# Kernel tuning notes

Hardware: AMD Instinct MI355X
Metric: run time of the kernel (lower is better)

The kernel has to match this reference:

```python
import jax, jax.numpy as jnp
import numpy as np

D = 1024      # EMBEDDING_DIM
H = 16        # ATTENTION_HEADS
HD = 64       # HEAD_DIM
B, S = 4, 2048
EPS = 1e-5


def setup_inputs() -> dict:
    key = jax.random.key(0)
    ks = jax.random.split(key, 16)
    std = 0.02
    inp = {
        "x": jax.random.normal(ks[0], (B, S, D), dtype=jnp.float32),
        # per-head Q/K/V weights stacked: [H, D, HD]
        "Wq": jax.random.normal(ks[1], (H, D, HD), dtype=jnp.float32) * std,
        "Wk": jax.random.normal(ks[2], (H, D, HD), dtype=jnp.float32) * std,
        "Wv": jax.random.normal(ks[3], (H, D, HD), dtype=jnp.float32) * std,
        "bq": jnp.zeros((H, HD), dtype=jnp.float32),
        "bk": jnp.zeros((H, HD), dtype=jnp.float32),
        "bv": jnp.zeros((H, HD), dtype=jnp.float32),
        "Wo": jax.random.normal(ks[4], (D, D), dtype=jnp.float32) * std,
        "bo": jnp.zeros((D,), dtype=jnp.float32),
        "W1": jax.random.normal(ks[5], (D, 4 * D), dtype=jnp.float32) * std,
        "b1": jnp.zeros((4 * D,), dtype=jnp.float32),
        "W2": jax.random.normal(ks[6], (4 * D, D), dtype=jnp.float32) * std,
        "b2": jnp.zeros((D,), dtype=jnp.float32),
        # single shared LayerNorm (same module used for both pre-norms)
        "gamma": jnp.ones((D,), dtype=jnp.float32),
        "beta": jnp.zeros((D,), dtype=jnp.float32),
    }
    return inp


def _layer_norm(x, gamma, beta):
    mu = jnp.mean(x, axis=-1, keepdims=True)
    var = jnp.mean(jnp.square(x - mu), axis=-1, keepdims=True)
    return (x - mu) * jax.lax.rsqrt(var + EPS) * gamma + beta


def _block(x, Wq, Wk, Wv, bq, bk, bv, Wo, bo, W1, b1, W2, b2, gamma, beta):
    # pre-norm attention
    h = _layer_norm(x, gamma, beta)                     # [B,S,D]
    Q = jnp.einsum('bsd,hdk->bhsk', h, Wq) + bq[None, :, None, :]
    K = jnp.einsum('bsd,hdk->bhsk', h, Wk) + bk[None, :, None, :]
    V = jnp.einsum('bsd,hdk->bhsk', h, Wv) + bv[None, :, None, :]
    scores = jnp.einsum('bhsk,bhtk->bhst', Q, K) / jnp.sqrt(jnp.float32(HD))
    causal = jnp.tril(jnp.ones((S, S), dtype=bool))     # True = keep
    scores = jnp.where(causal[None, None], scores, -jnp.inf)
    attn = jax.nn.softmax(scores, axis=-1)              # [B,H,S,S]
    out = jnp.einsum('bhst,bhtk->bhsk', attn, V)        # [B,H,S,HD]
    out = out.transpose(0, 2, 1, 3).reshape(x.shape[0], x.shape[1], D)
    x = x + out @ Wo + bo
    # pre-norm MLP (shared layer norm params)
    h2 = _layer_norm(x, gamma, beta)
    mlp = jax.nn.gelu(h2 @ W1 + b1, approximate=False) @ W2 + b2
    return x + mlp


def reference(x, Wq, Wk, Wv, bq, bk, bv, Wo, bo, W1, b1, W2, b2, gamma, beta):
    return _block(x, Wq, Wk, Wv, bq, bk, bv, Wo, bo, W1, b1, W2, b2, gamma, beta)
```

## Files before the change

kernel.cpp:

```cpp
#include <hip/hip_runtime.h>
#include <hip/hip_bf16.h>

typedef __bf16  bf16x8 __attribute__((ext_vector_type(8)));
typedef float   f32x4  __attribute__((ext_vector_type(4)));
typedef short   s16x8  __attribute__((ext_vector_type(8)));

typedef const __attribute__((address_space(1))) void g_void;
typedef __attribute__((address_space(3))) void l_void;

__device__ __forceinline__ short f2b(float x) {
    __hip_bfloat16 h = __float2bfloat16(x);
    return __builtin_bit_cast(short, h);
}

__device__ __forceinline__ int pk2(float lo, float hi) {
    return (int)(unsigned short)f2b(lo) | ((int)f2b(hi) << 16);
}

__device__ __forceinline__ float fast_gelu(float v) {
    const float a = fminf(2.3022082f * (v + 0.044715f * v * v * v), 126.0f);
    const float t = exp2f(a);
    return v * t / (t + 1.0f);
}

__device__ __forceinline__ f32x4 mfma16(s16x8 a, s16x8 b, f32x4 c) {
    return __builtin_amdgcn_mfma_f32_16x16x32_bf16(
        __builtin_bit_cast(bf16x8, a), __builtin_bit_cast(bf16x8, b), c, 0, 0, 0);
}

__global__ __launch_bounds__(256) void transpose_bf16(
    const float* __restrict__ src, short* __restrict__ dst, int R, int C) {
    __shared__ float tile[32][33];
    src += (size_t)blockIdx.z * R * C;
    dst += (size_t)blockIdx.z * R * C;
    const int c0 = blockIdx.x * 32, r0 = blockIdx.y * 32;
    const int tx = threadIdx.x & 31, ty = threadIdx.x >> 5;
#pragma unroll
    for (int i = 0; i < 32; i += 8)
        tile[ty + i][tx] = src[(size_t)(r0 + ty + i) * C + c0 + tx];
    __syncthreads();
#pragma unroll
    for (int i = 0; i < 32; i += 8)
        dst[(size_t)(c0 + ty + i) * R + r0 + tx] = f2b(tile[tx][ty + i]);
}

__global__ __launch_bounds__(256) void concat_bias(
    const float* __restrict__ bq, const float* __restrict__ bk,
    const float* __restrict__ bv, float* __restrict__ o) {
    int i = blockIdx.x * 256 + threadIdx.x;
    if (i < 1024)      o[i] = bq[i];
    else if (i < 2048) o[i] = bk[i - 1024];
    else if (i < 3072) o[i] = bv[i - 2048];
}

__global__ __launch_bounds__(256) void ln_bf16(
    const float* __restrict__ x, const float* __restrict__ gamma,
    const float* __restrict__ beta, short* __restrict__ out) {
    __shared__ float red[8];
    const int row = blockIdx.x, tid = threadIdx.x;
    const float4 v = *(const float4*)(x + (size_t)row * 1024 + tid * 4);
    float s = v.x + v.y + v.z + v.w;
    float q = v.x * v.x + v.y * v.y + v.z * v.z + v.w * v.w;
#pragma unroll
    for (int off = 32; off > 0; off >>= 1) {
        s += __shfl_xor(s, off);
        q += __shfl_xor(q, off);
    }
    if ((tid & 63) == 0) { red[(tid >> 6) * 2] = s; red[(tid >> 6) * 2 + 1] = q; }
    __syncthreads();
    s = red[0] + red[2] + red[4] + red[6];
    q = red[1] + red[3] + red[5] + red[7];
    const float mu = s * (1.0f / 1024.0f);
    const float var = q * (1.0f / 1024.0f) - mu * mu;
    const float rs = rsqrtf(var + 1e-5f);
    const float4 g  = *(const float4*)(gamma + tid * 4);
    const float4 bt = *(const float4*)(beta + tid * 4);
    short4 o;
    o.x = f2b((v.x - mu) * rs * g.x + bt.x);
    o.y = f2b((v.y - mu) * rs * g.y + bt.y);
    o.z = f2b((v.z - mu) * rs * g.z + bt.z);
    o.w = f2b((v.w - mu) * rs * g.w + bt.w);
    *(short4*)(out + (size_t)row * 1024 + tid * 4) = o;
}

template <int MODE, int SWZ>
__global__ __launch_bounds__(512) void gemm_bf16(
    const short* __restrict__ A, const short* __restrict__ Bt,
    const float* __restrict__ bias, const float* __restrict__ resid,
    float* __restrict__ outf, short* __restrict__ outb, short* __restrict__ vt,
    int M, int N, int K) {
    __shared__ __align__(16) short As[2 * 128 * 32];
    __shared__ __align__(16) short Bs[2 * 128 * 32];

    const int tid = threadIdx.x;
    const int wave = tid >> 6, lane = tid & 63;
    const int l16 = lane & 15, quad = lane >> 4;
    const int wm = wave & 3, wn = wave >> 2;
    const int gx = gridDim.x;
    const int g = blockIdx.y * gx + blockIdx.x;
    const int xcd = g & 7, s = g >> 3;
    int m0, n0;
    if (SWZ == 0) {
        const int nband = gx >> 3;
        const int sm = s / nband;
        const int sn = s - sm * nband;
        m0 = sm * 128;
        n0 = (xcd * nband + sn) * 128;
    } else {
        const int mband = gridDim.y >> 3;
        const int sm = s / gx;
        m0 = (xcd * mband + sm) * 128;
        n0 = (s - sm * gx) * 128;
    }
    const int lrow = lane >> 2;
    const int lcol = (lane & 3) * 8;

    f32x4 acc[2][4] = {};

    for (int kk = 0; kk < K; kk += 64) {
#pragma unroll
        for (int p = 0; p < 2; ++p) {
            const int r = wave * 16 + lrow;
            const short* ga = A + (size_t)(m0 + r) * K + kk + p * 32 + lcol;
            short* la = &As[p * 4096 + wave * 512];
            __builtin_amdgcn_global_load_lds((g_void*)ga, (l_void*)la, 16, 0, 0);
            const short* gb = Bt + (size_t)(n0 + r) * K + kk + p * 32 + lcol;
            short* lb = &Bs[p * 4096 + wave * 512];
            __builtin_amdgcn_global_load_lds((g_void*)gb, (l_void*)lb, 16, 0, 0);
        }
        __syncthreads();
#pragma unroll
        for (int p = 0; p < 2; ++p) {
            s16x8 a[2], b[4];
#pragma unroll
            for (int t = 0; t < 2; ++t)
                a[t] = *(const s16x8*)&As[p * 4096 + (wm * 32 + t * 16 + l16) * 32 + quad * 8];
#pragma unroll
            for (int t = 0; t < 4; ++t)
                b[t] = *(const s16x8*)&Bs[p * 4096 + (wn * 64 + t * 16 + l16) * 32 + quad * 8];
#pragma unroll
            for (int mt = 0; mt < 2; ++mt)
#pragma unroll
                for (int nt = 0; nt < 4; ++nt)
                    acc[mt][nt] = mfma16(a[mt], b[nt], acc[mt][nt]);
        }
        __syncthreads();
    }

#pragma unroll
    for (int mt = 0; mt < 2; ++mt) {
#pragma unroll
        for (int nt = 0; nt < 4; ++nt) {
            const int row = m0 + wm * 32 + mt * 16 + quad * 4;
            const int col = n0 + wn * 64 + nt * 16 + l16;
            const float bc = bias[col];
            float v[4];
#pragma unroll
            for (int r = 0; r < 4; ++r) v[r] = acc[mt][nt][r] + bc;

            if (MODE == 0) {
                const int sel = col >> 10, within = col & 1023;
                const int h = within >> 6, hd = within & 63;
                const size_t bidx = (size_t)row >> 11, sp = row & 2047;
                if (sel == 0) {
#pragma unroll
                    for (int r = 0; r < 4; ++r) v[r] *= 0.18033688011112042f;
                }
                if (sel < 2) {
#pragma unroll
                    for (int r = 0; r < 4; ++r)
                        outb[(size_t)sel * (8192ull * 1024) +
                             ((bidx * 16 + h) * 2048 + sp + r) * 64 + hd] = f2b(v[r]);
                } else {
                    short4 o4;
                    o4.x = f2b(v[0]); o4.y = f2b(v[1]);
                    o4.z = f2b(v[2]); o4.w = f2b(v[3]);
                    *(short4*)&vt[((bidx * 16 + h) * 64 + hd) * 2048 + sp] = o4;
                }
            } else if (MODE == 1) {
#pragma unroll
                for (int r = 0; r < 4; ++r) {
                    const size_t rr = (size_t)(row + r);
                    outf[rr * N + col] = v[r] + resid[rr * N + col];
                }
            } else {
#pragma unroll
                for (int r = 0; r < 4; ++r)
                    outb[(size_t)(row + r) * N + col] = f2b(fast_gelu(v[r]));
            }
        }
    }
}

__global__ __launch_bounds__(256) void attn_kernel(
    const short* __restrict__ Q, const short* __restrict__ K,
    const short* __restrict__ Vt, short* __restrict__ O) {
    const int bid = blockIdx.x;
    const int xcd = bid & 7;
    const int sub = (bid >> 3) & 7;
    const int grp = bid >> 6;
    const int bh  = grp * 8 + xcd;
    const int h = bh & 15, b = bh >> 4;
    const int gq = sub;
    const int tid = threadIdx.x, wave = tid >> 6, lane = tid & 63;
    const int l16 = lane & 15, quad = lane >> 4;

    __shared__ __align__(16) short Ks[2][64 * 72];
    __shared__ __align__(16) short Vts[2][64 * 72];
    __shared__ __align__(16) short Ps[4][16 * 72];

    const size_t bhoff = (size_t)bh * (2048ull * 64);
    const int srow = tid >> 2;
    const int sseg = (tid & 3) * 16;

    const int qts[4] = {gq, 15 - gq, 16 + gq, 31 - gq};

    for (int pass = 0; pass < 4; ++pass) {
        const int qt = qts[pass];
        const int q0 = qt * 64;
        const int q_lane = q0 + wave * 16 + l16;

        const short* qrow = Q + bhoff + (size_t)q_lane * 64;
        s16x8 bq0 = *(const s16x8*)(qrow + quad * 8);
        s16x8 bq1 = *(const s16x8*)(qrow + 32 + quad * 8);

        f32x4 oacc[4] = {};
        float lsum = 0.0f;

        s16x8 k0, k1, v0, v1;
        {
            const short* kg = K + bhoff + (size_t)srow * 64 + sseg;
            k0 = *(const s16x8*)kg;
            k1 = *(const s16x8*)(kg + 8);
            const short* vg = Vt + bhoff + (size_t)srow * 2048 + sseg;
            v0 = *(const s16x8*)vg;
            v1 = *(const s16x8*)(vg + 8);
        }

        for (int j = 0; j <= qt; ++j) {
            const int buf = j & 1;
            *(s16x8*)&Ks[buf][srow * 72 + sseg]      = k0;
            *(s16x8*)&Ks[buf][srow * 72 + sseg + 8]  = k1;
            *(s16x8*)&Vts[buf][srow * 72 + sseg]     = v0;
            *(s16x8*)&Vts[buf][srow * 72 + sseg + 8] = v1;
            __syncthreads();

            if (j < qt) {
                const short* kg = K + bhoff + (size_t)((j + 1) * 64 + srow) * 64 + sseg;
                k0 = *(const s16x8*)kg;
                k1 = *(const s16x8*)(kg + 8);
                const short* vg = Vt + bhoff + (size_t)srow * 2048 + (j + 1) * 64 + sseg;
                v0 = *(const s16x8*)vg;
                v1 = *(const s16x8*)(vg + 8);
            }

            f32x4 st[4];
#pragma unroll
            for (int s = 0; s < 4; ++s) {
                s16x8 ak0 = *(const s16x8*)&Ks[buf][(s * 16 + l16) * 72 + quad * 8];
                s16x8 ak1 = *(const s16x8*)&Ks[buf][(s * 16 + l16) * 72 + 32 + quad * 8];
                f32x4 c = {};
                c = mfma16(ak0, bq0, c);
                c = mfma16(ak1, bq1, c);
                st[s] = c;
            }
            if (j == qt) {
#pragma unroll
                for (int s = 0; s < 4; ++s)
#pragma unroll
                    for (int r = 0; r < 4; ++r) {
                        const int t = j * 64 + s * 16 + quad * 4 + r;
                        if (t > q_lane) st[s][r] = -3000.0f;
                    }
            }
            float rs = 0.0f;
#pragma unroll
            for (int s = 0; s < 4; ++s) {
#pragma unroll
                for (int r = 0; r < 4; ++r) {
                    st[s][r] = exp2f(st[s][r]);
                    rs += st[s][r];
                }
                int2 pw;
                pw.x = pk2(st[s][0], st[s][1]);
                pw.y = pk2(st[s][2], st[s][3]);
                *(int2*)&Ps[wave][l16 * 72 + s * 16 + quad * 4] = pw;
            }
            rs += __shfl_xor(rs, 16);
            rs += __shfl_xor(rs, 32);
            lsum += rs;

            asm volatile("s_waitcnt lgkmcnt(0)" ::: "memory");
            s16x8 ap0 = *(const s16x8*)&Ps[wave][l16 * 72 + quad * 8];
            s16x8 ap1 = *(const s16x8*)&Ps[wave][l16 * 72 + 32 + quad * 8];

#pragma unroll
            for (int nt = 0; nt < 4; ++nt) {
                s16x8 bv0 = *(const s16x8*)&Vts[buf][(nt * 16 + l16) * 72 + quad * 8];
                s16x8 bv1 = *(const s16x8*)&Vts[buf][(nt * 16 + l16) * 72 + 32 + quad * 8];
                oacc[nt] = mfma16(ap0, bv0, oacc[nt]);
                oacc[nt] = mfma16(ap1, bv1, oacc[nt]);
            }
        }
        __syncthreads();

        float inv[4];
#pragma unroll
        for (int r = 0; r < 4; ++r)
            inv[r] = 1.0f / __shfl(lsum, quad * 4 + r, 64);
#pragma unroll
        for (int nt = 0; nt < 4; ++nt)
#pragma unroll
            for (int r = 0; r < 4; ++r) {
                const int row = q0 + wave * 16 + quad * 4 + r;
                O[((size_t)b * 2048 + row) * 1024 + h * 64 + nt * 16 + l16] =
                    f2b(oacc[nt][r] * inv[r]);
            }
    }
}

extern "C" void kernel_launch(void* const* d_in, const int* in_sizes, int n_in,
                              void* d_out, int out_size, void* d_ws, size_t ws_size,
                              hipStream_t stream) {
    const float* x     = (const float*)d_in[0];
    const float* Wq    = (const float*)d_in[1];
    const float* Wk    = (const float*)d_in[2];
    const float* Wv    = (const float*)d_in[3];
    const float* bq    = (const float*)d_in[4];
    const float* bk    = (const float*)d_in[5];
    const float* bv    = (const float*)d_in[6];
    const float* Wo    = (const float*)d_in[7];
    const float* bo    = (const float*)d_in[8];
    const float* W1    = (const float*)d_in[9];
    const float* b1    = (const float*)d_in[10];
    const float* W2    = (const float*)d_in[11];
    const float* b2    = (const float*)d_in[12];
    const float* gamma = (const float*)d_in[13];
    const float* beta  = (const float*)d_in[14];
    float* out = (float*)d_out;

    char* ws = (char*)d_ws;
    size_t off = 0;
    auto alloc = [&](size_t bytes) -> char* {
        char* p = ws + off;
        off += (bytes + 255) & ~(size_t)255;
        return p;
    };
    short* h1    = (short*)alloc(8192ull * 1024 * 2);
    short* btqkv = (short*)alloc(3072ull * 1024 * 2);
    short* btwo  = (short*)alloc(1024ull * 1024 * 2);
    short* btw1  = (short*)alloc(4096ull * 1024 * 2);
    short* btw2  = (short*)alloc(1024ull * 4096 * 2);
    float* bqkv  = (float*)alloc(3072ull * 4);
    short* qkv   = (short*)alloc(2ull * 8192 * 1024 * 2);
    short* vt    = (short*)alloc(8192ull * 1024 * 2);
    short* aout  = (short*)alloc(8192ull * 1024 * 2);
    float* x2    = (float*)alloc(8192ull * 1024 * 4);
    short* h2    = (short*)alloc(8192ull * 1024 * 2);
    short* m1    = (short*)alloc(8192ull * 4096 * 2);

    transpose_bf16<<<dim3(2, 32, 16), 256, 0, stream>>>(Wq, btqkv, 1024, 64);
    transpose_bf16<<<dim3(2, 32, 16), 256, 0, stream>>>(Wk, btqkv + 1024ull * 1024, 1024, 64);
    transpose_bf16<<<dim3(2, 32, 16), 256, 0, stream>>>(Wv, btqkv + 2ull * 1024 * 1024, 1024, 64);
    transpose_bf16<<<dim3(32, 32, 1), 256, 0, stream>>>(Wo, btwo, 1024, 1024);
    transpose_bf16<<<dim3(128, 32, 1), 256, 0, stream>>>(W1, btw1, 1024, 4096);
    transpose_bf16<<<dim3(32, 128, 1), 256, 0, stream>>>(W2, btw2, 4096, 1024);
    concat_bias<<<12, 256, 0, stream>>>(bq, bk, bv, bqkv);

    ln_bf16<<<8192, 256, 0, stream>>>(x, gamma, beta, h1);
    gemm_bf16<0, 0><<<dim3(24, 64), 512, 0, stream>>>(
        h1, btqkv, bqkv, nullptr, nullptr, qkv, vt, 8192, 3072, 1024);
    attn_kernel<<<512, 256, 0, stream>>>(
        qkv, qkv + 8192ull * 1024, vt, aout);
    gemm_bf16<1, 0><<<dim3(8, 64), 512, 0, stream>>>(
        aout, btwo, bo, x, x2, nullptr, nullptr, 8192, 1024, 1024);
    ln_bf16<<<8192, 256, 0, stream>>>(x2, gamma, beta, h2);
    gemm_bf16<2, 0><<<dim3(32, 64), 512, 0, stream>>>(
        h2, btw1, b1, nullptr, nullptr, m1, nullptr, 8192, 4096, 1024);
    gemm_bf16<1, 1><<<dim3(8, 64), 512, 0, stream>>>(
        m1, btw2, b2, x2, out, nullptr, nullptr, 8192, 1024, 4096);
}
```

Before: 504.7 us.

## Add 256x256-tile pipelined GEMM kernel for QKV and MLP up-projection

Adds a new gemm256 kernel that computes 256x256 output tiles per 512-thread workgroup with 8x4 MFMA fragments per wave. It double-buffers A/B tiles in LDS using direct global-to-LDS loads with an XOR swizzle, and interleaves loads with MFMA phases using barriers and s_setprio. Workgroup ids are remapped across XCDs. The QKV projection and the W1+GELU GEMM now use it, aiming at more data reuse and better latency hiding, at the cost of higher register/LDS pressure and a fragile hand-scheduled pipeline.

```diff
diff --git a/kernel.cpp b/kernel.cpp
--- a/kernel.cpp
+++ b/kernel.cpp
@@ -158,6 +158,177 @@
 #pragma unroll
             for (int r = 0; r < 4; ++r) v[r] = acc[mt][nt][r] + bc;
 
+            if (MODE == 1) {
+#pragma unroll
+                for (int r = 0; r < 4; ++r) {
+                    const size_t rr = (size_t)(row + r);
+                    outf[rr * N + col] = v[r] + resid[rr * N + col];
+                }
+            } else {
+#pragma unroll
+                for (int r = 0; r < 4; ++r)
+                    outb[(size_t)(row + r) * N + col] = f2b(fast_gelu(v[r]));
+            }
+        }
+    }
+}
+
+
+#define MM(MH, NH, AF, BB)                                                   \
+    _Pragma("unroll") for (int p = 0; p < 2; ++p)                            \
+        _Pragma("unroll") for (int ii = 0; ii < 4; ++ii)                     \
+            _Pragma("unroll") for (int jj = 0; jj < 2; ++jj)                 \
+                acc[(MH) * 4 + ii][(NH) * 2 + jj] =                          \
+                    mfma16(AF[ii][p], BB[jj][p],                             \
+                           acc[(MH) * 4 + ii][(NH) * 2 + jj]);
+
+#define PH_MID                                                               \
+    __builtin_amdgcn_s_barrier();                                            \
+    __builtin_amdgcn_s_setprio(1);
+
+#define PH_END                                                               \
+    __builtin_amdgcn_s_setprio(0);                                           \
+    __builtin_amdgcn_sched_barrier(0);                                       \
+    __builtin_amdgcn_s_barrier();                                            \
+    __builtin_amdgcn_sched_barrier(0);
+
+#define KTILE(BUF, S1, S2, S3, S4)                                           \
+    {                                                                        \
+        s16x8 af[4][2], bl[2][2], bh[2][2];                                  \
+                                                     \
+        _Pragma("unroll") for (int ii = 0; ii < 4; ++ii)                     \
+            _Pragma("unroll") for (int p = 0; p < 2; ++p)                    \
+                af[ii][p] = LDA(BUF, ii, p);                                 \
+        _Pragma("unroll") for (int jj = 0; jj < 2; ++jj)                     \
+            _Pragma("unroll") for (int p = 0; p < 2; ++p)                    \
+                bl[jj][p] = LDB(BUF, jj, p);                                 \
+        S1;                                                                  \
+        PH_MID;                                                              \
+        MM(0, 0, af, bl);                                                    \
+        PH_END;                                                              \
+                                                     \
+        _Pragma("unroll") for (int jj = 0; jj < 2; ++jj)                     \
+            _Pragma("unroll") for (int p = 0; p < 2; ++p)                    \
+                bh[jj][p] = LDB(BUF, 2 + jj, p);                             \
+        S2;                                                                  \
+        PH_MID;                                                              \
+        MM(0, 1, af, bh);                                                    \
+        PH_END;                                                              \
+                                                     \
+        _Pragma("unroll") for (int ii = 0; ii < 4; ++ii)                     \
+            _Pragma("unroll") for (int p = 0; p < 2; ++p)                    \
+                af[ii][p] = LDA(BUF, 4 + ii, p);                             \
+        S3;                                                                  \
+        PH_MID;                                                              \
+        MM(1, 1, af, bh);                                                    \
+        PH_END;                                                              \
+                                      \
+        S4;                                                                  \
+        asm volatile("s_waitcnt vmcnt(4)" ::: "memory");                     \
+        PH_MID;                                                              \
+        MM(1, 0, af, bl);                                                    \
+        PH_END;                                                              \
+    }
+
+template <int MODE>
+__global__ __launch_bounds__(512, 2) void gemm256(
+    const short* __restrict__ A, const short* __restrict__ Bt,
+    const float* __restrict__ bias, const float* __restrict__ resid,
+    float* __restrict__ outf, short* __restrict__ outb, short* __restrict__ vt,
+    int M, int N, int K) {
+    __shared__ __align__(16) short As[32768];
+    __shared__ __align__(16) short Bs[32768];
+
+    const int tid = threadIdx.x;
+    const int wave = tid >> 6, lane = tid & 63;
+    const int l16 = lane & 15, quad = lane >> 4;
+    const int wm = wave >> 2, wn = wave & 3;
+
+    const int nwg = gridDim.x;
+    const int g = blockIdx.x;
+    const int wgid = (g & 7) * (nwg >> 3) + (g >> 3);
+    const int mtiles = M >> 8;
+    const int m0 = (wgid % mtiles) << 8;
+    const int n0 = (wgid / mtiles) << 8;
+
+    const int rc = l16 * 32 + ((quad * 8) ^ ((l16 >> 3) << 4));
+    const int a_rd = wm * 8192 + rc;
+    const int b_rd = (wn >> 1) * 8192 + (wn & 1) * 4096 + rc;
+
+    auto LDA = [&](int buf, int i, int p) {
+        return *(const s16x8*)&As[buf * 16384 + a_rd + (i * 2 + p) * 512];
+    };
+    auto LDB = [&](int buf, int j, int p) {
+        return *(const s16x8*)&Bs[buf * 16384 + b_rd + (j * 2 + p) * 512];
+    };
+
+    int r0, c0, r1, c1;
+    {
+        int s = tid * 16;
+        int lin = s ^ (((s >> 9) & 1) << 5);
+        r0 = ((lin >> 11) << 4) + ((lin >> 6) & 15);
+        c0 = (((lin >> 10) & 1) << 5) + ((lin & 63) >> 1);
+        s = (tid + 512) * 16;
+        lin = s ^ (((s >> 9) & 1) << 5);
+        r1 = ((lin >> 11) << 4) + ((lin >> 6) & 15);
+        c1 = (((lin >> 10) & 1) << 5) + ((lin & 63) >> 1);
+    }
+
+    const short* gA = A + (size_t)m0 * K;
+    const short* gB = Bt + (size_t)n0 * K;
+
+    auto STAGE = [&](const short* gbase, int half, int kk, short* lds) {
+        const short* s0 = gbase + (size_t)(half * 128 + r0) * K + kk + c0;
+        const short* s1 = gbase + (size_t)(half * 128 + r1) * K + kk + c1;
+        short* d0 = lds + half * 8192 + wave * 512;
+        short* d1 = lds + half * 8192 + 4096 + wave * 512;
+        __builtin_amdgcn_global_load_lds((g_void*)s0, (l_void*)d0, 16, 0, 0);
+        __builtin_amdgcn_global_load_lds((g_void*)s1, (l_void*)d1, 16, 0, 0);
+    };
+
+    f32x4 acc[8][4] = {};
+
+    STAGE(gA, 0, 0, As);
+    STAGE(gA, 1, 0, As);
+    STAGE(gB, 0, 0, Bs);
+    STAGE(gB, 1, 0, Bs);
+    STAGE(gB, 0, 64, Bs + 16384);
+    STAGE(gB, 1, 64, Bs + 16384);
+    asm volatile("s_waitcnt vmcnt(4)" ::: "memory");
+    __builtin_amdgcn_s_barrier();
+    __builtin_amdgcn_sched_barrier(0);
+
+    const int NI = K >> 7;
+    for (int it = 0; it < NI; ++it) {
+        const int kA1 = (2 * it + 1) * 64;
+        int kn0 = (2 * it + 2) * 64;
+        if (kn0 > K - 64) kn0 = K - 64;
+        int kn1 = (2 * it + 3) * 64;
+        if (kn1 > K - 64) kn1 = K - 64;
+
+        KTILE(0,
+              STAGE(gA, 0, kA1, As + 16384),
+              STAGE(gA, 1, kA1, As + 16384),
+              STAGE(gB, 0, kn0, Bs),
+              STAGE(gB, 1, kn0, Bs));
+        KTILE(1,
+              STAGE(gA, 0, kn0, As),
+              STAGE(gA, 1, kn0, As),
+              STAGE(gB, 0, kn1, Bs + 16384),
+              STAGE(gB, 1, kn1, Bs + 16384));
+    }
+
+#pragma unroll
+    for (int i = 0; i < 8; ++i) {
+#pragma unroll
+        for (int j = 0; j < 4; ++j) {
+            const int row = m0 + wm * 128 + i * 16 + quad * 4;
+            const int col = n0 + wn * 64 + j * 16 + l16;
+            const float bc = bias[col];
+            float v[4];
+#pragma unroll
+            for (int r = 0; r < 4; ++r) v[r] = acc[i][j][r] + bc;
+
             if (MODE == 0) {
                 const int sel = col >> 10, within = col & 1023;
                 const int h = within >> 6, hd = within & 63;
@@ -191,6 +362,11 @@
         }
     }
 }
+
+#undef KTILE
+#undef PH_MID
+#undef PH_END
+#undef MM
 
 __global__ __launch_bounds__(256) void attn_kernel(
     const short* __restrict__ Q, const short* __restrict__ K,
@@ -368,14 +544,14 @@
     concat_bias<<<12, 256, 0, stream>>>(bq, bk, bv, bqkv);
 
     ln_bf16<<<8192, 256, 0, stream>>>(x, gamma, beta, h1);
-    gemm_bf16<0, 0><<<dim3(24, 64), 512, 0, stream>>>(
+    gemm256<0><<<384, 512, 0, stream>>>(
         h1, btqkv, bqkv, nullptr, nullptr, qkv, vt, 8192, 3072, 1024);
     attn_kernel<<<512, 256, 0, stream>>>(
         qkv, qkv + 8192ull * 1024, vt, aout);
     gemm_bf16<1, 0><<<dim3(8, 64), 512, 0, stream>>>(
         aout, btwo, bo, x, x2, nullptr, nullptr, 8192, 1024, 1024);
     ln_bf16<<<8192, 256, 0, stream>>>(x2, gamma, beta, h2);
-    gemm_bf16<2, 0><<<dim3(32, 64), 512, 0, stream>>>(
+    gemm256<2><<<512, 512, 0, stream>>>(
         h2, btw1, b1, nullptr, nullptr, m1, nullptr, 8192, 4096, 1024);
     gemm_bf16<1, 1><<<dim3(8, 64), 512, 0, stream>>>(
         m1, btw2, b2, x2, out, nullptr, nullptr, 8192, 1024, 4096);
```

Measured after the change: 531.1 us. 1.05x slower.

## Add 256x256 bf16 GEMM with direct-to-LDS loads for QKV and MLP-up

Applied to the files above, without the earlier changes.

Adds a new GEMM kernel that computes 256x256 output tiles per 512-thread workgroup. It loads A and B straight from global memory into LDS, double-buffers the K loop, and software-pipelines inline-asm ds_read_b128 fragment loads against MFMA chains with wave priority raised during the MFMA bursts. Block indices are remapped so that consecutive tiles are spread over XCDs. The QKV projection and the first MLP GEMM now use this kernel, aiming for more operand reuse and better latency hiding; the cost is 128KB of LDS per block, limiting occupancy to one block per CU, plus hand-tuned waitcnt logic that is fragile.

```diff
diff --git a/kernel.cpp b/kernel.cpp
--- a/kernel.cpp
+++ b/kernel.cpp
@@ -4,6 +4,7 @@
 typedef __bf16  bf16x8 __attribute__((ext_vector_type(8)));
 typedef float   f32x4  __attribute__((ext_vector_type(4)));
 typedef short   s16x8  __attribute__((ext_vector_type(8)));
+typedef int     i32x4  __attribute__((ext_vector_type(4)));
 
 typedef const __attribute__((address_space(1))) void g_void;
 typedef __attribute__((address_space(3))) void l_void;
@@ -27,6 +28,8 @@
     return __builtin_amdgcn_mfma_f32_16x16x32_bf16(
         __builtin_bit_cast(bf16x8, a), __builtin_bit_cast(bf16x8, b), c, 0, 0, 0);
 }
+
+#define S16(x) __builtin_bit_cast(s16x8, x)
 
 __global__ __launch_bounds__(256) void transpose_bf16(
     const float* __restrict__ src, short* __restrict__ dst, int R, int C) {
@@ -158,6 +161,197 @@
 #pragma unroll
             for (int r = 0; r < 4; ++r) v[r] = acc[mt][nt][r] + bc;
 
+            if (MODE == 1) {
+#pragma unroll
+                for (int r = 0; r < 4; ++r) {
+                    const size_t rr = (size_t)(row + r);
+                    outf[rr * N + col] = v[r] + resid[rr * N + col];
+                }
+            } else {
+#pragma unroll
+                for (int r = 0; r < 4; ++r)
+                    outb[(size_t)(row + r) * N + col] = f2b(fast_gelu(v[r]));
+            }
+        }
+    }
+}
+
+
+#define DSR(dst, b, o)                                                       \
+    asm volatile("ds_read_b128 %0, %1 offset:" #o : "=v"(dst) : "v"(b))
+
+#define LGKM12                                                               \
+    asm volatile("s_waitcnt lgkmcnt(12)" ::: "memory");                      \
+    __builtin_amdgcn_sched_barrier(0)
+
+#define MM32(A, B)                                                           \
+    acc[0][0]=mfma16(S16(A##0),S16(B##0),acc[0][0]);                         \
+    acc[0][1]=mfma16(S16(A##0),S16(B##1),acc[0][1]);                         \
+    acc[0][2]=mfma16(S16(A##0),S16(B##2),acc[0][2]);                         \
+    acc[0][3]=mfma16(S16(A##0),S16(B##3),acc[0][3]);                         \
+    acc[1][0]=mfma16(S16(A##1),S16(B##0),acc[1][0]);                         \
+    acc[1][1]=mfma16(S16(A##1),S16(B##1),acc[1][1]);                         \
+    acc[1][2]=mfma16(S16(A##1),S16(B##2),acc[1][2]);                         \
+    acc[1][3]=mfma16(S16(A##1),S16(B##3),acc[1][3]);                         \
+    acc[2][0]=mfma16(S16(A##2),S16(B##0),acc[2][0]);                         \
+    acc[2][1]=mfma16(S16(A##2),S16(B##1),acc[2][1]);                         \
+    acc[2][2]=mfma16(S16(A##2),S16(B##2),acc[2][2]);                         \
+    acc[2][3]=mfma16(S16(A##2),S16(B##3),acc[2][3]);                         \
+    acc[3][0]=mfma16(S16(A##3),S16(B##0),acc[3][0]);                         \
+    acc[3][1]=mfma16(S16(A##3),S16(B##1),acc[3][1]);                         \
+    acc[3][2]=mfma16(S16(A##3),S16(B##2),acc[3][2]);                         \
+    acc[3][3]=mfma16(S16(A##3),S16(B##3),acc[3][3]);                         \
+    acc[4][0]=mfma16(S16(A##4),S16(B##0),acc[4][0]);                         \
+    acc[4][1]=mfma16(S16(A##4),S16(B##1),acc[4][1]);                         \
+    acc[4][2]=mfma16(S16(A##4),S16(B##2),acc[4][2]);                         \
+    acc[4][3]=mfma16(S16(A##4),S16(B##3),acc[4][3]);                         \
+    acc[5][0]=mfma16(S16(A##5),S16(B##0),acc[5][0]);                         \
+    acc[5][1]=mfma16(S16(A##5),S16(B##1),acc[5][1]);                         \
+    acc[5][2]=mfma16(S16(A##5),S16(B##2),acc[5][2]);                         \
+    acc[5][3]=mfma16(S16(A##5),S16(B##3),acc[5][3]);                         \
+    acc[6][0]=mfma16(S16(A##6),S16(B##0),acc[6][0]);                         \
+    acc[6][1]=mfma16(S16(A##6),S16(B##1),acc[6][1]);                         \
+    acc[6][2]=mfma16(S16(A##6),S16(B##2),acc[6][2]);                         \
+    acc[6][3]=mfma16(S16(A##6),S16(B##3),acc[6][3]);                         \
+    acc[7][0]=mfma16(S16(A##7),S16(B##0),acc[7][0]);                         \
+    acc[7][1]=mfma16(S16(A##7),S16(B##1),acc[7][1]);                         \
+    acc[7][2]=mfma16(S16(A##7),S16(B##2),acc[7][2]);                         \
+    acc[7][3]=mfma16(S16(A##7),S16(B##3),acc[7][3])
+
+#define READ_P0(SA, SB, AR, BR)                                              \
+    DSR(SB##0, BR, 0);    DSR(SB##1, BR, 2048);                              \
+    DSR(SB##2, BR, 4096); DSR(SB##3, BR, 6144);                              \
+    DSR(SA##0, AR, 0);    DSR(SA##1, AR, 2048);                              \
+    DSR(SA##2, AR, 4096); DSR(SA##3, AR, 6144);                              \
+    DSR(SA##4, AR, 8192); DSR(SA##5, AR, 10240);                             \
+    DSR(SA##6, AR, 12288); DSR(SA##7, AR, 14336)
+
+#define READ_P1(SA, SB, AR, BR)                                              \
+    DSR(SB##0, BR, 1024); DSR(SB##1, BR, 3072);                              \
+    DSR(SB##2, BR, 5120); DSR(SB##3, BR, 7168);                              \
+    DSR(SA##0, AR, 1024); DSR(SA##1, AR, 3072);                              \
+    DSR(SA##2, AR, 5120); DSR(SA##3, AR, 7168);                              \
+    DSR(SA##4, AR, 9216); DSR(SA##5, AR, 11264);                             \
+    DSR(SA##6, AR, 13312); DSR(SA##7, AR, 15360)
+
+#define TILE(ARc, BRc, ARn, BRn, BUFB)                                       \
+    READ_P1(ga, gb, ARc, BRc);                                               \
+    LGKM12;                                                                  \
+    __builtin_amdgcn_s_setprio(1);                                           \
+    MM32(fa, fb);                                                            \
+    __builtin_amdgcn_s_setprio(0);                                           \
+    __builtin_amdgcn_sched_barrier(0);                                       \
+    READ_P0(fa, fb, ARn, BRn);                                               \
+    LGKM12;                                                                  \
+    STAGE8(BUFB);                                                            \
+    __builtin_amdgcn_s_setprio(1);                                           \
+    MM32(ga, gb);                                                            \
+    __builtin_amdgcn_s_setprio(0);                                           \
+    __builtin_amdgcn_sched_barrier(0);                                       \
+    ADV();                                                                   \
+    asm volatile("s_waitcnt vmcnt(8)" ::: "memory");                         \
+    __builtin_amdgcn_s_barrier();                                            \
+    __builtin_amdgcn_sched_barrier(0)
+
+template <int MODE>
+__global__ __launch_bounds__(512, 2) void gemm256(
+    const short* __restrict__ A, const short* __restrict__ Bt,
+    const float* __restrict__ bias, const float* __restrict__ resid,
+    float* __restrict__ outf, short* __restrict__ outb, short* __restrict__ vt,
+    int M, int N, int K) {
+    __shared__ __align__(16) short As[32768];
+    __shared__ __align__(16) short Bs[32768];
+
+    const int tid = threadIdx.x;
+    const int wave = tid >> 6, lane = tid & 63;
+    const int l16 = lane & 15, quad = lane >> 4;
+    const int wm = wave >> 2, wn = wave & 3;
+
+    const int nwg = gridDim.x;
+    const int g = blockIdx.x;
+    const int wgid = (g & 7) * (nwg >> 3) + (g >> 3);
+    const int mtiles = M >> 8;
+    const int m0 = (wgid % mtiles) << 8;
+    const int n0 = (wgid / mtiles) << 8;
+
+    const int rc = l16 * 32 + ((quad * 8) ^ ((l16 >> 3) << 4));
+    const int a_rd = wm * 8192 + rc;
+    const int b_rd = (wn >> 1) * 8192 + (wn & 1) * 4096 + rc;
+
+    const uint32_t asb = (uint32_t)(uintptr_t)(l_void*)&As[0];
+    const uint32_t bsb = (uint32_t)(uintptr_t)(l_void*)&Bs[0];
+    const uint32_t aRd0 = asb + 2u * (uint32_t)a_rd, aRd1 = aRd0 + 32768u;
+    const uint32_t bRd0 = bsb + 2u * (uint32_t)b_rd, bRd1 = bRd0 + 32768u;
+
+    int r0, c0, r1, c1;
+    {
+        int s = tid * 16;
+        int lin = s ^ (((s >> 9) & 1) << 5);
+        r0 = ((lin >> 11) << 4) + ((lin >> 6) & 15);
+        c0 = (((lin >> 10) & 1) << 5) + ((lin & 63) >> 1);
+        s = (tid + 512) * 16;
+        lin = s ^ (((s >> 9) & 1) << 5);
+        r1 = ((lin >> 11) << 4) + ((lin >> 6) & 15);
+        c1 = (((lin >> 10) & 1) << 5) + ((lin & 63) >> 1);
+    }
+
+    const short* pa00 = A + (size_t)(m0 + r0) * K + c0;
+    const short* pa01 = A + (size_t)(m0 + r1) * K + c1;
+    const short* pa10 = A + (size_t)(m0 + 128 + r0) * K + c0;
+    const short* pa11 = A + (size_t)(m0 + 128 + r1) * K + c1;
+    const short* pb00 = Bt + (size_t)(n0 + r0) * K + c0;
+    const short* pb01 = Bt + (size_t)(n0 + r1) * K + c1;
+    const short* pb10 = Bt + (size_t)(n0 + 128 + r0) * K + c0;
+    const short* pb11 = Bt + (size_t)(n0 + 128 + r1) * K + c1;
+
+    short* lA = &As[0];
+    short* lB = &Bs[0];
+    const int wv512 = wave * 512;
+
+    auto STAGE8 = [&](int bufsh) {
+        __builtin_amdgcn_global_load_lds((g_void*)pa00, (l_void*)(lA + bufsh + wv512), 16, 0, 0);
+        __builtin_amdgcn_global_load_lds((g_void*)pa01, (l_void*)(lA + bufsh + 4096 + wv512), 16, 0, 0);
+        __builtin_amdgcn_global_load_lds((g_void*)pa10, (l_void*)(lA + bufsh + 8192 + wv512), 16, 0, 0);
+        __builtin_amdgcn_global_load_lds((g_void*)pa11, (l_void*)(lA + bufsh + 12288 + wv512), 16, 0, 0);
+        __builtin_amdgcn_global_load_lds((g_void*)pb00, (l_void*)(lB + bufsh + wv512), 16, 0, 0);
+        __builtin_amdgcn_global_load_lds((g_void*)pb01, (l_void*)(lB + bufsh + 4096 + wv512), 16, 0, 0);
+        __builtin_amdgcn_global_load_lds((g_void*)pb10, (l_void*)(lB + bufsh + 8192 + wv512), 16, 0, 0);
+        __builtin_amdgcn_global_load_lds((g_void*)pb11, (l_void*)(lB + bufsh + 12288 + wv512), 16, 0, 0);
+    };
+    auto ADV = [&]() {
+        pa00 += 64; pa01 += 64; pa10 += 64; pa11 += 64;
+        pb00 += 64; pb01 += 64; pb10 += 64; pb11 += 64;
+    };
+
+    f32x4 acc[8][4] = {};
+    i32x4 fa0, fa1, fa2, fa3, fa4, fa5, fa6, fa7, fb0, fb1, fb2, fb3;
+    i32x4 ga0, ga1, ga2, ga3, ga4, ga5, ga6, ga7, gb0, gb1, gb2, gb3;
+
+    STAGE8(0);      ADV();
+    STAGE8(16384);  ADV();
+    asm volatile("s_waitcnt vmcnt(0)" ::: "memory");
+    __builtin_amdgcn_s_barrier();
+    __builtin_amdgcn_sched_barrier(0);
+    READ_P0(fa, fb, aRd0, bRd0);
+
+    const int NT = K >> 6;
+    for (int it = 0; it < NT; it += 2) {
+        TILE(aRd0, bRd0, aRd1, bRd1, 0);
+        TILE(aRd1, bRd1, aRd0, bRd0, 16384);
+    }
+    asm volatile("s_waitcnt vmcnt(0) lgkmcnt(0)" ::: "memory");
+
+#pragma unroll
+    for (int i = 0; i < 8; ++i) {
+#pragma unroll
+        for (int j = 0; j < 4; ++j) {
+            const int row = m0 + wm * 128 + i * 16 + quad * 4;
+            const int col = n0 + wn * 64 + j * 16 + l16;
+            const float bc = bias[col];
+            float v[4];
+#pragma unroll
+            for (int r = 0; r < 4; ++r) v[r] = acc[i][j][r] + bc;
+
             if (MODE == 0) {
                 const int sel = col >> 10, within = col & 1023;
                 const int h = within >> 6, hd = within & 63;
@@ -191,6 +385,13 @@
         }
     }
 }
+
+#undef TILE
+#undef READ_P0
+#undef READ_P1
+#undef MM32
+#undef LGKM12
+#undef DSR
 
 __global__ __launch_bounds__(256) void attn_kernel(
     const short* __restrict__ Q, const short* __restrict__ K,
@@ -368,14 +569,14 @@
     concat_bias<<<12, 256, 0, stream>>>(bq, bk, bv, bqkv);
 
     ln_bf16<<<8192, 256, 0, stream>>>(x, gamma, beta, h1);
-    gemm_bf16<0, 0><<<dim3(24, 64), 512, 0, stream>>>(
+    gemm256<0><<<384, 512, 0, stream>>>(
         h1, btqkv, bqkv, nullptr, nullptr, qkv, vt, 8192, 3072, 1024);
     attn_kernel<<<512, 256, 0, stream>>>(
         qkv, qkv + 8192ull * 1024, vt, aout);
     gemm_bf16<1, 0><<<dim3(8, 64), 512, 0, stream>>>(
         aout, btwo, bo, x, x2, nullptr, nullptr, 8192, 1024, 1024);
     ln_bf16<<<8192, 256, 0, stream>>>(x2, gamma, beta, h2);
-    gemm_bf16<2, 0><<<dim3(32, 64), 512, 0, stream>>>(
+    gemm256<2><<<512, 512, 0, stream>>>(
         h2, btw1, b1, nullptr, nullptr, m1, nullptr, 8192, 4096, 1024);
     gemm_bf16<1, 1><<<dim3(8, 64), 512, 0, stream>>>(
         m1, btw2, b2, x2, out, nullptr, nullptr, 8192, 1024, 4096);
```

After: 699.4 us. 1.39x slower.
